# Kernel optimization log

Measured on AMD Instinct MI355X. Metric: run time of the kernel, lower is better.

## Reference

```python
import jax, jax.numpy as jnp
import numpy as np

T = 4                 # number of spiking timesteps (module init T)
NUM_THRESHOLDS = 8    # K thresholds: thresh / 2**k
B, C, H, W = 32, 128, 32, 32


def setup_inputs() -> dict:
    key = jax.random.key(0)
    x = jax.random.normal(key, ((T + 1) * B, C, H, W), dtype=jnp.float32)
    thresh = jnp.ones((1,), dtype=jnp.float32)
    return {"x": x, "thresh": thresh}


def _forward(x, thresh):
    # ExpandTemporalDim(T+1): [(T+1)*B, C, H, W] -> [T+1, B, C, H, W]
    xt_all = x.reshape((T + 1, B, C, H, W))
    # thre_shaped: [K, 1, 1, 1, 1]
    time_steps = (2.0 ** jnp.arange(NUM_THRESHOLDS, dtype=jnp.float32)).reshape(
        (NUM_THRESHOLDS, 1, 1, 1, 1))
    thre = thresh / time_steps
    thre_thr = thre * 0.75
    bias = xt_all[0]

    def step(carry, inp):
        mem, cum, exp_in, exp_out = carry
        xt, t = inp
        mem = mem + xt - bias + exp_in - exp_out
        cum = cum + exp_out
        # [K, B, C, H, W] indicator tensors
        pos = (mem[None] >= thre_thr).astype(jnp.float32)
        neg = ((mem[None] <= -thre_thr).astype(jnp.float32)
               * (cum[None] >= thre).astype(jnp.float32))
        # pos_true[0] = pos[0]; pos_true[k] = pos[k] - pos[k-1]
        zk = jnp.zeros_like(pos[:1])
        pos_true = jnp.diff(pos, axis=0, prepend=zk)
        neg_true = jnp.diff(neg, axis=0, prepend=zk)
        spike = (jnp.sum(thre * pos_true, axis=0)
                 - jnp.sum(thre * neg_true, axis=0))
        mem = mem - spike
        cum = cum + spike
        denom = t + 1.0
        exp_in = exp_in + (xt - bias) / denom
        exp_out = exp_out + spike / denom
        return (mem, cum, exp_in, exp_out), spike

    z = jnp.zeros_like(bias)
    carry0 = (z, z, bias, z)  # mem=0, cumulative_out=0, exp_in=x[0], exp_out=0
    ts = jnp.arange(T, dtype=jnp.float32)
    _, spikes = jax.lax.scan(step, carry0, (xt_all[1:], ts))
    # spike_pot[0] is zeros, then the T spikes; MergeTemporalDim flattens back
    out = jnp.concatenate([z[None], spikes], axis=0)
    return out.reshape(((T + 1) * B, C, H, W))


def reference(x, thresh):
    return _forward(x, thresh)
```

## Files before the change

### kernel.cpp

```cpp
#include <hip/hip_runtime.h>


constexpr int T_STEPS = 4;
constexpr int K_THR   = 8;

__global__ __launch_bounds__(256) void mth_kernel(
    const float* __restrict__ x, const float* __restrict__ thresh,
    float* __restrict__ out, int n4)
{
    const float th = thresh[0];
    const int i = blockIdx.x * blockDim.x + threadIdx.x;
    if (i >= n4) return;

    const float4* __restrict__ xv = reinterpret_cast<const float4*>(x);
    float4* __restrict__ ov       = reinterpret_cast<float4*>(out);

    const float4 b4 = xv[i];
    ov[i] = make_float4(0.f, 0.f, 0.f, 0.f);

    float b[4]    = {b4.x, b4.y, b4.z, b4.w};
    float mem[4]  = {0.f, 0.f, 0.f, 0.f};
    float cum[4]  = {0.f, 0.f, 0.f, 0.f};
    float ein[4]  = {b4.x, b4.y, b4.z, b4.w};
    float eout[4] = {0.f, 0.f, 0.f, 0.f};

    #pragma unroll
    for (int t = 0; t < T_STEPS; ++t) {
        const float4 x4 = xv[(size_t)(t + 1) * n4 + i];
        const float xt[4] = {x4.x, x4.y, x4.z, x4.w};
        const float denom = (float)(t + 1);
        float sp[4];

        #pragma unroll
        for (int j = 0; j < 4; ++j) {
            mem[j] = mem[j] + xt[j] - b[j] + ein[j] - eout[j];
            cum[j] = cum[j] + eout[j];

            float spike = 0.f, pos_prev = 0.f, neg_prev = 0.f;
            #pragma unroll
            for (int k = 0; k < K_THR; ++k) {
                const float thre = th * (1.0f / (float)(1 << k));
                const float tt   = 0.75f * thre;
                const float pos  = (mem[j] >= tt) ? 1.f : 0.f;
                const float neg  = (mem[j] <= -tt && cum[j] >= thre) ? 1.f : 0.f;
                spike = spike + thre * (pos - pos_prev) - thre * (neg - neg_prev);
                pos_prev = pos;
                neg_prev = neg;
            }

            mem[j]  = mem[j] - spike;
            cum[j]  = cum[j] + spike;
            ein[j]  = ein[j] + (xt[j] - b[j]) / denom;
            eout[j] = eout[j] + spike / denom;
            sp[j]   = spike;
        }

        ov[(size_t)(t + 1) * n4 + i] = make_float4(sp[0], sp[1], sp[2], sp[3]);
    }
}

extern "C" void kernel_launch(void* const* d_in, const int* in_sizes, int n_in,
                              void* d_out, int out_size, void* d_ws, size_t ws_size,
                              hipStream_t stream)
{
    const float* x      = (const float*)d_in[0];
    const float* thresh = (const float*)d_in[1];
    float* out          = (float*)d_out;

    const int N  = in_sizes[0] / (T_STEPS + 1);
    const int n4 = N / 4;

    const int block = 256;
    const int grid  = (n4 + block - 1) / block;
    mth_kernel<<<grid, block, 0, stream>>>(x, thresh, out, n4);
}
```

Baseline: 150.2 us.

## Hoist loads, simplify threshold loop, use nontemporal stores

Issues all five input float4 loads up front so they are in flight together, and precomputes the threshold tables. The telescoping pos/neg difference sum is replaced by a select of the highest crossed threshold. The per-step division is replaced by constant multiplies, and outputs are written with nontemporal stores to avoid polluting cache. Results could differ slightly because of reassociation and the changed division, and the early loads raise register pressure.

New measurement: 152.0 us. About the same (+1.2%).

```diff
diff --git a/kernel.cpp b/kernel.cpp
--- a/kernel.cpp
+++ b/kernel.cpp
@@ -4,19 +4,35 @@
 constexpr int T_STEPS = 4;
 constexpr int K_THR   = 8;
 
+typedef float f32x4 __attribute__((ext_vector_type(4)));
+
 __global__ __launch_bounds__(256) void mth_kernel(
     const float* __restrict__ x, const float* __restrict__ thresh,
     float* __restrict__ out, int n4)
 {
-    const float th = thresh[0];
+    const float th = __uint_as_float(
+        __builtin_amdgcn_readfirstlane(__float_as_uint(thresh[0])));
+
     const int i = blockIdx.x * blockDim.x + threadIdx.x;
     if (i >= n4) return;
 
-    const float4* __restrict__ xv = reinterpret_cast<const float4*>(x);
-    float4* __restrict__ ov       = reinterpret_cast<float4*>(out);
+    const f32x4* __restrict__ xv = reinterpret_cast<const f32x4*>(x);
+    f32x4* __restrict__ ov       = reinterpret_cast<f32x4*>(out);
 
-    const float4 b4 = xv[i];
-    ov[i] = make_float4(0.f, 0.f, 0.f, 0.f);
+    float thre[K_THR], tt[K_THR];
+    #pragma unroll
+    for (int k = 0; k < K_THR; ++k) {
+        thre[k] = th * (1.0f / (float)(1 << k));
+        tt[k]   = 0.75f * thre[k];
+    }
+
+    const f32x4 b4 = xv[i];
+    f32x4 xt4[T_STEPS];
+    #pragma unroll
+    for (int t = 0; t < T_STEPS; ++t)
+        xt4[t] = xv[(size_t)(t + 1) * n4 + i];
+
+    __builtin_nontemporal_store((f32x4){0.f, 0.f, 0.f, 0.f}, &ov[i]);
 
     float b[4]    = {b4.x, b4.y, b4.z, b4.w};
     float mem[4]  = {0.f, 0.f, 0.f, 0.f};
@@ -26,36 +42,34 @@
 
     #pragma unroll
     for (int t = 0; t < T_STEPS; ++t) {
-        const float4 x4 = xv[(size_t)(t + 1) * n4 + i];
-        const float xt[4] = {x4.x, x4.y, x4.z, x4.w};
-        const float denom = (float)(t + 1);
-        float sp[4];
+        const float xt[4] = {xt4[t].x, xt4[t].y, xt4[t].z, xt4[t].w};
+        f32x4 sp4;
 
         #pragma unroll
         for (int j = 0; j < 4; ++j) {
-            mem[j] = mem[j] + xt[j] - b[j] + ein[j] - eout[j];
-            cum[j] = cum[j] + eout[j];
+            float m = (((mem[j] + xt[j]) - b[j]) + ein[j]) - eout[j];
+            float c = cum[j] + eout[j];
 
-            float spike = 0.f, pos_prev = 0.f, neg_prev = 0.f;
+            float sp = 0.f, sn = 0.f;
             #pragma unroll
-            for (int k = 0; k < K_THR; ++k) {
-                const float thre = th * (1.0f / (float)(1 << k));
-                const float tt   = 0.75f * thre;
-                const float pos  = (mem[j] >= tt) ? 1.f : 0.f;
-                const float neg  = (mem[j] <= -tt && cum[j] >= thre) ? 1.f : 0.f;
-                spike = spike + thre * (pos - pos_prev) - thre * (neg - neg_prev);
-                pos_prev = pos;
-                neg_prev = neg;
+            for (int k = K_THR - 1; k >= 0; --k) {
+                sp = (m >= tt[k]) ? thre[k] : sp;
+                sn = (m <= -tt[k] && c >= thre[k]) ? thre[k] : sn;
             }
+            const float spike = sp - sn;
 
-            mem[j]  = mem[j] - spike;
-            cum[j]  = cum[j] + spike;
-            ein[j]  = ein[j] + (xt[j] - b[j]) / denom;
-            eout[j] = eout[j] + spike / denom;
-            sp[j]   = spike;
+            m -= spike;
+            c += spike;
+            const float d = xt[j] - b[j];
+            if (t == 0)      { ein[j] += d;         eout[j] += spike;         }
+            else if (t == 1) { ein[j] += d * 0.5f;  eout[j] += spike * 0.5f;  }
+            else if (t == 2) { ein[j] += d / 3.0f;  eout[j] += spike / 3.0f;  }
+            else             { ein[j] += d * 0.25f; eout[j] += spike * 0.25f; }
+
+            mem[j] = m; cum[j] = c; sp4[j] = spike;
         }
 
-        ov[(size_t)(t + 1) * n4 + i] = make_float4(sp[0], sp[1], sp[2], sp[3]);
+        __builtin_nontemporal_store(sp4, &ov[(size_t)(t + 1) * n4 + i]);
     }
 }
 
```
